# Kernel tuning notes

Measured on AMD Instinct MI355X. Metric: run time of the kernel, lower is better.

## Reference

```python
import jax, jax.numpy as jnp
import numpy as np

EPS = 1e-5
GROUPS = 8


def conv2d(x, w, b, pad):
    y = jax.lax.conv_general_dilated(
        x, w, window_strides=(1, 1), padding=[(pad, pad), (pad, pad)],
        dimension_numbers=('NCHW', 'OIHW', 'NCHW'))
    return y + b[None, :, None, None]


def setup_inputs() -> dict:
    key = jax.random.key(0)
    ks = jax.random.split(key, 8)
    b, c, h, w = 32, 256, 56, 56
    cg = c // GROUPS
    x = jax.random.normal(ks[0], (b, c, h, w), dtype=jnp.float32)
    w1 = jax.random.normal(ks[1], (cg, cg, 1, 1), dtype=jnp.float32) * 0.05
    b1 = jnp.zeros((cg,), dtype=jnp.float32)
    w3a = jax.random.normal(ks[2], (cg, cg, 3, 3), dtype=jnp.float32) * 0.05
    b3a = jnp.zeros((cg,), dtype=jnp.float32)
    w3b = jax.random.normal(ks[3], (c, c, 3, 3), dtype=jnp.float32) * 0.02
    b3b = jnp.zeros((c,), dtype=jnp.float32)
    gn_w = jnp.ones((cg,), dtype=jnp.float32)
    gn_b = jnp.zeros((cg,), dtype=jnp.float32)
    return {"x": x, "w1": w1, "b1": b1, "w3a": w3a, "b3a": b3a,
            "w3b": w3b, "b3b": b3b, "gn_w": gn_w, "gn_b": gn_b}


def reference(x, w1, b1, w3a, b3a, w3b, b3b, gn_w, gn_b):
    b, c, h, w = x.shape
    cg = c // GROUPS
    bg = b * GROUPS
    gx = x.reshape(bg, cg, h, w)

    # spatial attention on grouped channels
    x_h = gx.mean(axis=3, keepdims=True)                       # [bg,cg,h,1]
    x_w = gx.mean(axis=2, keepdims=True).transpose(0, 1, 3, 2)  # [bg,cg,w,1]
    hw = conv2d(jnp.concatenate([x_h, x_w], axis=2), w1, b1, 0)
    xh, xw = hw[:, :, :h], hw[:, :, h:]
    x0 = gx * jax.nn.sigmoid(xh) * jax.nn.sigmoid(xw.transpose(0, 1, 3, 2))

    # GroupNorm with num_groups == num_channels (per-channel over HxW)
    mu = x0.mean(axis=(2, 3), keepdims=True)
    var = x0.var(axis=(2, 3), keepdims=True)
    x1 = (x0 - mu) / jnp.sqrt(var + EPS) * gn_w[None, :, None, None] + gn_b[None, :, None, None]

    x2 = conv2d(gx, w3a, b3a, 1)

    # channel softmax-matmul attention (per group)
    x11 = jax.nn.softmax(x1.mean(axis=(2, 3)), axis=-1)[:, None, :]  # [bg,1,cg]
    x12 = x1.reshape(bg, cg, h * w)
    x21 = jax.nn.softmax(x2.mean(axis=(2, 3)), axis=-1)[:, None, :]
    x22 = x2.reshape(bg, cg, h * w)
    weights1 = (jnp.matmul(x11, x22) + jnp.matmul(x21, x12)).reshape(bg, 1, h, w)

    # BatchNorm2d(affine=False), batch statistics (training mode)
    xr = x0.reshape(b, c, h, w)
    bm = xr.mean(axis=(0, 2, 3), keepdims=True)
    bv = xr.var(axis=(0, 2, 3), keepdims=True)
    x3 = (xr - bm) / jnp.sqrt(bv + EPS)

    x4 = conv2d(x, w3b, b3b, 1)

    # spatial softmax-matmul attention over full channels
    x31 = jax.nn.softmax(x3.mean(axis=1).reshape(b, 1, h * w), axis=-1)  # [b,1,hw]
    x32 = x3.reshape(b, c, h * w).transpose(0, 2, 1)                     # [b,hw,c]
    x41 = jax.nn.softmax(x4.mean(axis=1).reshape(b, 1, h * w), axis=-1)
    x42 = x4.reshape(b, c, h * w).transpose(0, 2, 1)
    weights2 = (jnp.matmul(x31, x42) + jnp.matmul(x41, x32)).reshape(b, c, 1, 1)

    return (gx * jax.nn.sigmoid(weights1)).reshape(b, c, h, w) + x * jax.nn.sigmoid(weights2)
```

## Files before the change

kernel.cpp:

```cpp
#include <hip/hip_runtime.h>
#include <math.h>

#define B  32
#define C  256
#define HH 56
#define WW 56
#define HW 3136
#define G  8
#define CG 32
#define BG 256
#define GC 8192
#define EPSF 1e-5f

typedef __attribute__((ext_vector_type(8))) short short8;
typedef __attribute__((ext_vector_type(4))) float f32x4;

#define GLOAD16(g, l) __builtin_amdgcn_global_load_lds( \
    (const __attribute__((address_space(1))) void*)(g), \
    (__attribute__((address_space(3))) void*)(l), 16, 0, 0)

__device__ __forceinline__ float sigmoidf_(float v){ return 1.0f/(1.0f+__expf(-v)); }
__device__ __forceinline__ unsigned short f2bf(float v){
  unsigned u = __builtin_bit_cast(unsigned, v);
  u = u + 0x7FFFu + ((u>>16)&1u);
  return (unsigned short)(u>>16);
}
__device__ __forceinline__ float bf2f(unsigned short v){
  return __builtin_bit_cast(float, ((unsigned)v)<<16);
}

__global__ __launch_bounds__(256) void k1x(const float* __restrict__ x, unsigned short* __restrict__ xt,
    float* __restrict__ rowm, float* __restrict__ colm){
  int bid = blockIdx.x;
  int b = bid>>4; int icb = (bid>>1)&7; int rh = bid&1;
  __shared__ float tile[32][57];
  __shared__ float colacc[32][56];
  int tid = threadIdx.x;
  for(int e=tid; e<1792; e+=256) colacc[e/56][e%56] = 0.f;
  __syncthreads();
  const float* xb = x + ((size_t)b*256 + icb*32)*HW;
  for(int ii=0; ii<28; ++ii){
    int i = rh*28 + ii;
    for(int e=tid; e<1792; e+=256){
      int ch=e/56, j=e%56;
      tile[ch][j] = xb[(size_t)ch*HW + i*56 + j];
    }
    __syncthreads();
    if(tid<32){
      float s=0.f;
      #pragma unroll 8
      for(int j=0;j<56;j++) s += tile[tid][j];
      rowm[((size_t)b*256 + icb*32 + tid)*56 + i] = s*(1.0f/56.0f);
    }
    for(int e=tid; e<1792; e+=256){
      int ch=e/56, j=e%56;
      colacc[ch][j] += tile[ch][j];
    }
    if(tid<224){
      int j = tid>>2, k = tid&3;
      short8 v;
      #pragma unroll
      for(int m=0;m<8;m++) v[m] = (short)f2bf(tile[k*8+m][j]);
      *(short8*)(xt + (((size_t)b*58 + i+1)*58 + (j+1))*256 + icb*32 + k*8) = v;
    }
    __syncthreads();
  }
  for(int e=tid; e<1792; e+=256){
    int ch=e/56, j=e%56;
    atomicAdd(&colm[((size_t)b*256+icb*32+ch)*56 + j], colacc[ch][j]);
  }
}

__global__ void khalo(unsigned short* __restrict__ xt){
  int bid = blockIdx.x;
  int b = bid/228, hp = bid%228;
  int pi, pj;
  if(hp<58){pi=0;pj=hp;}
  else if(hp<116){pi=57;pj=hp-58;}
  else if(hp<172){pi=hp-116+1;pj=0;}
  else {pi=hp-172+1;pj=57;}
  xt[(((size_t)b*58+pi)*58+pj)*256 + threadIdx.x] = 0;
}

__global__ void k2_hw(const float* __restrict__ rowm, const float* __restrict__ colm,
                      const float* __restrict__ w1, const float* __restrict__ b1,
                      float* __restrict__ sh, float* __restrict__ sw,
                      float* __restrict__ shT, float* __restrict__ swT){
  int bg = blockIdx.x;
  int b = bg>>3, g = bg&7;
  __shared__ float inb[32][112];
  __shared__ float wt[32*32];
  __shared__ float bb[32];
  for(int idx=threadIdx.x; idx<32*56; idx+=blockDim.x){
    int ic=idx/56, p=idx%56;
    inb[ic][p]    = rowm[(bg*32+ic)*56+p];
    inb[ic][56+p] = colm[(bg*32+ic)*56+p]*(1.0f/56.0f);
  }
  for(int idx=threadIdx.x; idx<1024; idx+=blockDim.x) wt[idx]=w1[idx];
  if(threadIdx.x<32) bb[threadIdx.x]=b1[threadIdx.x];
  __syncthreads();
  for(int o=threadIdx.x; o<32*112; o+=blockDim.x){
    int oc=o/112, p=o%112;
    float s=bb[oc];
    #pragma unroll
    for(int ic=0;ic<32;ic++) s += wt[oc*32+ic]*inb[ic][p];
    float sg = sigmoidf_(s);
    int c = g*32+oc;
    if(p<56){
      sh[(bg*32+oc)*56+p]=sg;
      shT[((size_t)b*56+p)*256 + c]=sg;
    } else {
      sw[(bg*32+oc)*56+(p-56)]=sg;
      swT[((size_t)b*56+(p-56))*256 + c]=sg;
    }
  }
}

__global__ void k2b_x11(const float* __restrict__ gnb, const float* __restrict__ b3a, float* __restrict__ x11){
  __shared__ float v[32];
  if(threadIdx.x<32) v[threadIdx.x]=gnb[threadIdx.x];
  __syncthreads();
  if(threadIdx.x==0){
    float m=-1e30f; for(int i=0;i<32;i++) m=fmaxf(m,v[i]);
    float s=0.f; for(int i=0;i<32;i++){ v[i]=__expf(v[i]-m); s+=v[i]; }
    float d=0.f;
    for(int i=0;i<32;i++){ float p=v[i]/s; x11[i]=p; d+=p*b3a[i]; }
    x11[32]=d;
  }
}

__global__ void k3_stats(const float* __restrict__ x, const float* __restrict__ sh, const float* __restrict__ sw,
                         float* __restrict__ gsum, float* __restrict__ gsq){
  int gc=blockIdx.x;
  __shared__ float ssh[56], ssw[56];
  if(threadIdx.x<56) ssh[threadIdx.x]=sh[gc*56+threadIdx.x];
  else if(threadIdx.x>=64&&threadIdx.x<120) ssw[threadIdx.x-64]=sw[gc*56+threadIdx.x-64];
  __syncthreads();
  const float* xp=x+(size_t)gc*HW;
  float s=0.f,s2=0.f;
  for(int p=threadIdx.x;p<HW;p+=blockDim.x){
    float v=xp[p]*ssh[p/56]*ssw[p%56];
    s+=v; s2+=v*v;
  }
  for(int off=32;off>0;off>>=1){ s+=__shfl_down(s,off,64); s2+=__shfl_down(s2,off,64); }
  __shared__ float rs[4], rs2[4];
  int wid=threadIdx.x>>6, lane=threadIdx.x&63;
  if(lane==0){rs[wid]=s; rs2[wid]=s2;}
  __syncthreads();
  if(threadIdx.x==0){
    gsum[gc]=rs[0]+rs[1]+rs[2]+rs[3];
    gsq[gc]=rs2[0]+rs2[1]+rs2[2]+rs2[3];
  }
}

__global__ void k4a(const float* __restrict__ gsum, const float* __restrict__ gsq,
                    float* __restrict__ mu, float* __restrict__ istd){
  int gc=blockIdx.x*256+threadIdx.x;
  float m=gsum[gc]*(1.0f/HW);
  float v=gsq[gc]*(1.0f/HW)-m*m;
  mu[gc]=m; istd[gc]=rsqrtf(v+EPSF);
}

__global__ void k4b(const float* __restrict__ gsum, const float* __restrict__ gsq,
                    float* __restrict__ bm, float* __restrict__ binv){
  int c=threadIdx.x;
  float s=0.f,s2=0.f;
  for(int b=0;b<B;b++){ s+=gsum[b*256+c]; s2+=gsq[b*256+c]; }
  float m=s*(1.0f/(B*HW));
  float v=s2*(1.0f/(B*HW))-m*m;
  bm[c]=m; binv[c]=rsqrtf(v+EPSF);
}

__global__ __launch_bounds__(128) void k5m(const unsigned short* __restrict__ xt,
    const unsigned short* __restrict__ wta, const float* __restrict__ x11,
    float* __restrict__ w1a, float* __restrict__ cs2){
  __shared__ short Bs[6*58*32];
  int bid = blockIdx.x;
  int xcd = bid & 7; int idx = bid >> 3;
  int b = xcd + 8*(idx/112); int idx2 = idx % 112;
  int g = idx2 / 14; int pt = idx2 % 14;
  int bg = b*8 + g;
  int i0 = pt*4;
  int tid = threadIdx.x;
  int lane = tid & 63, wv = tid >> 6;
  int q = lane >> 4, rl = lane & 15;
  const unsigned short* xb = xt + (size_t)b*58*58*256 + g*32;

  #pragma unroll
  for(int issue=0; issue<11; ++issue){
    int idxl = issue*128 + tid;
    if(idxl < 1392){
      int pl = idxl >> 2, ch = idxl & 3;
      int r = pl / 58, jj = pl - r*58;
      const unsigned short* src = xb + ((size_t)(i0 + r)*58 + jj)*256 + ((ch ^ ((pl>>1)&3))<<3);
      GLOAD16(src, &Bs[idxl*8]);
    }
  }
  __syncthreads();

  f32x4 acc[2][7];
  #pragma unroll
  for(int mi=0;mi<2;mi++)
    #pragma unroll
    for(int ni=0;ni<7;ni++) acc[mi][ni]=(f32x4){0.f,0.f,0.f,0.f};

  int pr[7], pj[7];
  #pragma unroll
  for(int ni=0;ni<7;ni++){
    int px = wv*112 + ni*16 + rl;
    pr[ni] = px/56; pj[ni] = px - pr[ni]*56;
  }

  for(int tap=0; tap<9; ++tap){
    int dy = tap/3, dx = tap - dy*3;
    short8 a[2], bfr[7];
    #pragma unroll
    for(int mi=0;mi<2;mi++)
      a[mi] = *(const short8*)(wta + tap*1024 + (mi*16+rl)*32 + q*8);
    #pragma unroll
    for(int ni=0;ni<7;ni++){
      int pix = (pr[ni] + dy)*58 + pj[ni] + dx;
      int cs = q ^ ((pix>>1)&3);
      bfr[ni] = *(const short8*)&Bs[pix*32 + cs*8];
    }
    #pragma unroll
    for(int mi=0;mi<2;mi++)
      #pragma unroll
      for(int ni=0;ni<7;ni++)
        acc[mi][ni] = __builtin_amdgcn_mfma_f32_16x16x32_bf16(a[mi], bfr[ni], acc[mi][ni], 0,0,0);
  }

  float x11v[2][4];
  #pragma unroll
  for(int mi=0;mi<2;mi++)
    #pragma unroll
    for(int r=0;r<4;r++) x11v[mi][r] = x11[mi*16 + q*4 + r];
  float x11b = x11[32];
  size_t pxg0 = (size_t)bg*HW + i0*56 + wv*112;
  #pragma unroll
  for(int ni=0;ni<7;ni++){
    float s=0.f;
    #pragma unroll
    for(int mi=0;mi<2;mi++)
      #pragma unroll
      for(int r=0;r<4;r++) s += x11v[mi][r]*acc[mi][ni][r];
    s += __shfl_xor(s,16,64);
    s += __shfl_xor(s,32,64);
    if(lane<16) w1a[pxg0 + ni*16 + lane] = s + x11b;
  }
  #pragma unroll
  for(int mi=0;mi<2;mi++){
    #pragma unroll
    for(int r=0;r<4;r++){
      float s=0.f;
      #pragma unroll
      for(int ni=0;ni<7;ni++) s += acc[mi][ni][r];
      s += __shfl_xor(s,1,64);
      s += __shfl_xor(s,2,64);
      s += __shfl_xor(s,4,64);
      s += __shfl_xor(s,8,64);
      if(rl==0) atomicAdd(&cs2[bg*32 + mi*16 + q*4 + r], s);
    }
  }
}

__global__ void k6(const float* __restrict__ cs2, const float* __restrict__ b3a,
                   const float* __restrict__ mu, const float* __restrict__ istd,
                   const float* __restrict__ gnw, const float* __restrict__ gnb,
                   float* __restrict__ av, float* __restrict__ cst){
  int bg=blockIdx.x; int t=threadIdx.x;
  float m = cs2[bg*32+t]*(1.0f/HW) + b3a[t];
  float mx=m;
  for(int off=16;off>0;off>>=1) mx=fmaxf(mx,__shfl_xor(mx,off,32));
  float e=__expf(m-mx);
  float s=e;
  for(int off=16;off>0;off>>=1) s+=__shfl_xor(s,off,32);
  float x21=e/s;
  int gc=bg*32+t;
  float is=istd[gc];
  av[gc]=x21*is*gnw[t];
  float cv=x21*(gnb[t]-mu[gc]*is*gnw[t]);
  for(int off=16;off>0;off>>=1) cv+=__shfl_xor(cv,off,32);
  if(t==0) cst[bg]=cv;
}

__global__ __launch_bounds__(256) void k7x(const unsigned short* __restrict__ xt,
    const float* __restrict__ shT, const float* __restrict__ swT,
    const float* __restrict__ av, const float* __restrict__ binv, const float* __restrict__ cst,
    const float* __restrict__ w1a, float* __restrict__ sg1, float* __restrict__ s3pre){
  int bid = blockIdx.x; int b = bid/56, i = bid%56;
  __shared__ float shs[256], avs[256], bins[256], cst8[8];
  int tid = threadIdx.x;
  shs[tid]  = shT[((size_t)b*56+i)*256 + tid];
  avs[tid]  = av[b*256 + tid];
  bins[tid] = binv[tid];
  if(tid<8) cst8[tid] = cst[b*8+tid];
  __syncthreads();
  int h = tid>>5, l = tid&31;
  int bg = l>>2;
  int c0 = l*8;
  float sh8[8], av8[8], bi8[8];
  #pragma unroll
  for(int m=0;m<8;m++){ sh8[m]=shs[c0+m]; av8[m]=avs[c0+m]; bi8[m]=bins[c0+m]; }
  float cstv = cst8[bg];
  for(int pass=0; pass<7; ++pass){
    int j = pass*8 + h;
    short8 xv = *(const short8*)(xt + (((size_t)b*58 + i+1)*58 + j+1)*256 + c0);
    const float* swp = swT + ((size_t)b*56 + j)*256 + c0;
    float ws=0.f, s3=0.f;
    #pragma unroll
    for(int m=0;m<8;m++){
      float x0 = bf2f((unsigned short)xv[m]) * sh8[m] * swp[m];
      ws += av8[m]*x0;
      s3 += bi8[m]*x0;
    }
    ws += __shfl_xor(ws,1,64);
    ws += __shfl_xor(ws,2,64);
    s3 += __shfl_xor(s3,1,64);
    s3 += __shfl_xor(s3,2,64);
    s3 += __shfl_xor(s3,4,64);
    s3 += __shfl_xor(s3,8,64);
    s3 += __shfl_xor(s3,16,64);
    int p = i*56 + j;
    if((l&3)==0){
      size_t o = ((size_t)(b*8+bg))*HW + p;
      sg1[o] = sigmoidf_(w1a[o] + ws + cstv);
    }
    if(l==0) s3pre[(size_t)b*HW + p] = s3*(1.0f/256.0f);
  }
}

__global__ void k_softmax_hw(const float* __restrict__ in, float* __restrict__ out, float scale){
  int b=blockIdx.x;
  const float* ip=in+(size_t)b*HW;
  float mx=-1e30f;
  for(int p=threadIdx.x;p<HW;p+=blockDim.x) mx=fmaxf(mx,ip[p]*scale);
  for(int off=32;off>0;off>>=1) mx=fmaxf(mx,__shfl_xor(mx,off,64));
  __shared__ float red[8];
  int wid=threadIdx.x>>6, lane=threadIdx.x&63;
  if(lane==0) red[wid]=mx;
  __syncthreads();
  mx=red[0];
  #pragma unroll
  for(int w=1;w<8;w++) mx=fmaxf(mx,red[w]);
  float s=0.f;
  for(int p=threadIdx.x;p<HW;p+=blockDim.x) s+=__expf(ip[p]*scale-mx);
  for(int off=32;off>0;off>>=1) s+=__shfl_down(s,off,64);
  __shared__ float red2[8];
  if(lane==0) red2[wid]=s;
  __syncthreads();
  s=red2[0];
  #pragma unroll
  for(int w=1;w<8;w++) s+=red2[w];
  float inv=1.0f/s;
  for(int p=threadIdx.x;p<HW;p+=blockDim.x) out[(size_t)b*HW+p]=__expf(ip[p]*scale-mx)*inv;
}

__global__ void kwt(const float* __restrict__ w3b, unsigned short* __restrict__ wt){
  int idx = blockIdx.x*256 + threadIdx.x;
  int tap = idx >> 16; int r = idx & 65535; int oc = r >> 8; int ic = r & 255;
  wt[idx] = f2bf(w3b[((size_t)oc*256 + ic)*9 + tap]);
}

__global__ void kwta(const float* __restrict__ w3a, unsigned short* __restrict__ wta){
  int idx = blockIdx.x*256 + threadIdx.x;
  if(idx < 9216){
    int tap = idx >> 10; int r = idx & 1023; int oc = r >> 5; int ic = r & 31;
    wta[idx] = f2bf(w3a[((size_t)oc*32 + ic)*9 + tap]);
  }
}

__global__ __launch_bounds__(512) void k9m(const unsigned short* __restrict__ xt,
    const unsigned short* __restrict__ wt, const float* __restrict__ x31,
    float* __restrict__ s4pre, float* __restrict__ w2a){
  __shared__ short Ab[2][128*32];
  __shared__ short Bb[2][224*32];
  int bid = blockIdx.x;
  int xcd = bid & 7; int idx = bid >> 3;
  int b = xcd + 8*(idx/28); int rr = idx % 28;
  int pt = rr >> 1; int oct = rr & 1;
  int i0 = pt*4; int ocb = oct*128;
  int tid = threadIdx.x;
  int lane = tid & 63, wv = tid >> 6;
  int wm = wv & 3, wn = wv >> 2;
  int q = lane >> 4, rl = lane & 15;
  const unsigned short* xb = xt + (size_t)b*58*58*256;

  #define STAGE_A(BUF, TAP, IC0) do{ \
    int idxl = tid; int oc_ = idxl>>2, cs_ = idxl&3; \
    const unsigned short* src = wt + (((size_t)(TAP)*256 + ocb + oc_)*256 + (IC0) + (((cs_ ^ ((oc_>>1)&3)))<<3)); \
    GLOAD16(src, &Ab[BUF][idxl*8]); }while(0)
  #define STAGE_B(BUF, TAP, IC0) do{ \
    int dy_ = (TAP)/3, dx_ = (TAP)%3; \
    { int idxl = tid; int px_ = idxl>>2, cs_ = idxl&3; int r_ = px_/56, j_ = px_ - r_*56; \
      const unsigned short* src = xb + ((size_t)((i0 + r_ + dy_)*58 + (j_ + dx_)))*256 + (IC0) + ((cs_ ^ ((px_>>1)&3))<<3); \
      GLOAD16(src, &Bb[BUF][idxl*8]); } \
    if(tid < 384){ int idxl = tid + 512; int px_ = idxl>>2, cs_ = idxl&3; int r_ = px_/56, j_ = px_ - r_*56; \
      const unsigned short* src = xb + ((size_t)((i0 + r_ + dy_)*58 + (j_ + dx_)))*256 + (IC0) + ((cs_ ^ ((px_>>1)&3))<<3); \
      GLOAD16(src, &Bb[BUF][idxl*8]); } }while(0)

  STAGE_A(0, 0, 0);
  STAGE_B(0, 0, 0);
  __syncthreads();

  f32x4 acc[2][7];
  #pragma unroll
  for(int mi=0;mi<2;mi++)
    #pragma unroll
    for(int ni=0;ni<7;ni++) acc[mi][ni] = (f32x4){0.f,0.f,0.f,0.f};

  for(int t=0; t<72; ++t){
    int cur = t & 1;
    if(t+1 < 72){
      int tn = t+1; int tap = tn >> 3; int ic0 = (tn & 7) << 5;
      STAGE_A(cur^1, tap, ic0);
      STAGE_B(cur^1, tap, ic0);
    }
    short8 a[2], bf[7];
    #pragma unroll
    for(int mi=0;mi<2;mi++){
      int row = wm*32 + mi*16 + rl;
      int cs = q ^ ((row>>1)&3);
      a[mi] = *(const short8*)&Ab[cur][row*32 + cs*8];
    }
    #pragma unroll
    for(int ni=0;ni<7;ni++){
      int px = wn*112 + ni*16 + rl;
      int cs = q ^ ((px>>1)&3);
      bf[ni] = *(const short8*)&Bb[cur][px*32 + cs*8];
    }
    #pragma unroll
    for(int mi=0;mi<2;mi++)
      #pragma unroll
      for(int ni=0;ni<7;ni++)
        acc[mi][ni] = __builtin_amdgcn_mfma_f32_16x16x32_bf16(a[mi], bf[ni], acc[mi][ni], 0,0,0);
    __syncthreads();
  }
  #undef STAGE_A
  #undef STAGE_B

  size_t pxbase = (size_t)b*HW + i0*56 + wn*112;
  #pragma unroll
  for(int ni=0;ni<7;ni++){
    float s = 0.f;
    #pragma unroll
    for(int mi=0;mi<2;mi++){
      s += acc[mi][ni][0]+acc[mi][ni][1]+acc[mi][ni][2]+acc[mi][ni][3];
    }
    s += __shfl_xor(s, 16, 64);
    s += __shfl_xor(s, 32, 64);
    if(lane < 16) atomicAdd(&s4pre[pxbase + ni*16 + lane], s);
  }
  float x31v[7];
  #pragma unroll
  for(int ni=0;ni<7;ni++) x31v[ni] = x31[pxbase + ni*16 + rl];
  #pragma unroll
  for(int mi=0;mi<2;mi++){
    #pragma unroll
    for(int r=0;r<4;r++){
      float s = 0.f;
      #pragma unroll
      for(int ni=0;ni<7;ni++) s += x31v[ni]*acc[mi][ni][r];
      s += __shfl_xor(s, 1, 64);
      s += __shfl_xor(s, 2, 64);
      s += __shfl_xor(s, 4, 64);
      s += __shfl_xor(s, 8, 64);
      if(rl == 0) atomicAdd(&w2a[b*256 + ocb + wm*32 + mi*16 + q*4 + r], s);
    }
  }
}

__global__ __launch_bounds__(256) void k11f(const float* __restrict__ x, const float* __restrict__ sh,
    const float* __restrict__ sw, const float* __restrict__ x41, const float* __restrict__ bm,
    const float* __restrict__ binv, const float* __restrict__ w2a, const float* __restrict__ b3b,
    const float* __restrict__ sg1, float* __restrict__ out){
  int gc=blockIdx.x; int b=gc>>8, c=gc&255, bg=gc>>5;
  __shared__ float xs[HW];
  __shared__ float ssh[56], ssw[56];
  __shared__ float red[4];
  int tid=threadIdx.x;
  if(tid<56) ssh[tid]=sh[gc*56+tid];
  else if(tid>=64&&tid<120) ssw[tid-64]=sw[gc*56+tid-64];
  const float* xp=x+(size_t)gc*HW;
  const float* wp=x41+(size_t)b*HW;
  for(int p=tid;p<HW;p+=256) xs[p]=xp[p];
  __syncthreads();
  float s=0.f;
  for(int p=tid;p<HW;p+=256){
    float x0=xs[p]*ssh[p/56]*ssw[p%56];
    s+=wp[p]*x0;
  }
  for(int off=32;off>0;off>>=1) s+=__shfl_down(s,off,64);
  int wid=tid>>6, lane=tid&63;
  if(lane==0) red[wid]=s;
  __syncthreads();
  float t=red[0]+red[1]+red[2]+red[3];
  float sg2=sigmoidf_(w2a[gc]+b3b[c]+binv[c]*t-bm[c]*binv[c]);
  const float* sp=sg1+(size_t)bg*HW;
  float* op=out+(size_t)gc*HW;
  for(int p=tid;p<HW;p+=256){
    op[p]=xs[p]*(sp[p]+sg2);
  }
}

extern "C" void kernel_launch(void* const* d_in, const int* in_sizes, int n_in,
                              void* d_out, int out_size, void* d_ws, size_t ws_size,
                              hipStream_t stream) {
  const float* x   = (const float*)d_in[0];
  const float* w1  = (const float*)d_in[1];
  const float* b1  = (const float*)d_in[2];
  const float* w3a = (const float*)d_in[3];
  const float* b3a = (const float*)d_in[4];
  const float* w3b = (const float*)d_in[5];
  const float* b3b = (const float*)d_in[6];
  const float* gnw = (const float*)d_in[7];
  const float* gnb = (const float*)d_in[8];
  float* out=(float*)d_out;
  float* ws=(float*)d_ws;

  float* rowm=ws;
  float* colm=rowm+458752;
  float* sh  =colm+458752;
  float* sw  =sh+458752;
  float* x11 =sw+458752;
  float* gsum=x11+64;
  float* gsq =gsum+8192;
  float* mu  =gsq+8192;
  float* istd=mu+8192;
  float* bm  =istd+8192;
  float* binv=bm+256;
  float* cs2 =binv+256;
  float* w1a =cs2+8192;
  float* av  =w1a+802816;
  float* cst =av+8192;
  float* s3  =cst+256;
  float* x31 =s3+100352;
  float* s4  =x31+100352;
  float* x41 =s4+100352;
  float* w2a =x41+100352;
  float* shT =w2a+8192;
  float* swT =shT+458752;
  float* sg1 =swT+458752;
  unsigned short* xt = (unsigned short*)(sg1 + 802816);
  unsigned short* wtb = xt + (size_t)32*58*58*256;
  unsigned short* wta = wtb + 589824;

  hipMemsetAsync(colm, 0, 458752*sizeof(float), stream);
  k1x<<<512,256,0,stream>>>(x, xt, rowm, colm);
  khalo<<<32*228,256,0,stream>>>(xt);
  kwt<<<2304,256,0,stream>>>(w3b, wtb);
  kwta<<<36,256,0,stream>>>(w3a, wta);

  k2_hw<<<BG,128,0,stream>>>(rowm,colm,w1,b1,sh,sw,shT,swT);
  k2b_x11<<<1,32,0,stream>>>(gnb,b3a,x11);
  k3_stats<<<GC,256,0,stream>>>(x,sh,sw,gsum,gsq);
  k4a<<<32,256,0,stream>>>(gsum,gsq,mu,istd);
  k4b<<<1,256,0,stream>>>(gsum,gsq,bm,binv);
  hipMemsetAsync(cs2,0,8192*sizeof(float),stream);
  k5m<<<256*14,128,0,stream>>>(xt,wta,x11,w1a,cs2);
  k6<<<BG,32,0,stream>>>(cs2,b3a,mu,istd,gnw,gnb,av,cst);
  k7x<<<B*56,256,0,stream>>>(xt,shT,swT,av,binv,cst,w1a,sg1,s3);
  k_softmax_hw<<<B,512,0,stream>>>(s3,x31,1.0f);
  hipMemsetAsync(w2a,0,8192*sizeof(float),stream);
  hipMemsetAsync(s4,0,(size_t)HW*B*sizeof(float),stream);
  k9m<<<32*28,512,0,stream>>>(xt,wtb,x31,s4,w2a);
  k_softmax_hw<<<B,512,0,stream>>>(s4,x41,1.0f/256.0f);
  k11f<<<GC,256,0,stream>>>(x,sh,sw,x41,bm,binv,w2a,b3b,sg1,out);
}
```

Baseline: 415.5 us.

## Split fused transpose/row-col-mean kernel into separate highly parallel kernels

Replaces the single 512-block kernel, which looped over rows to build the bf16 NHWC padded copy and row/column means with atomics, with two kernels. A tiled 64x64 transpose kernel launches 6272 blocks to write the bf16 copy, and a per-channel kernel (8192 blocks) computes row and column means directly without atomics or a memset. The aim is more parallelism and no serial loop or atomic traffic, at the cost of reading x twice from memory and scalar 2-byte stores in the transpose.

After: 357.1 us. 1.16x faster.

```diff
diff --git a/kernel.cpp b/kernel.cpp
--- a/kernel.cpp
+++ b/kernel.cpp
@@ -29,45 +29,45 @@
   return __builtin_bit_cast(float, ((unsigned)v)<<16);
 }
 
-__global__ __launch_bounds__(256) void k1x(const float* __restrict__ x, unsigned short* __restrict__ xt,
-    float* __restrict__ rowm, float* __restrict__ colm){
+__global__ void k1_rowcol(const float* __restrict__ x, float* __restrict__ rowm, float* __restrict__ colm){
+  int gc = blockIdx.x;
+  __shared__ float t[56][57];
+  const float* xp = x + (size_t)gc*HW;
+  for(int idx=threadIdx.x; idx<HW; idx+=blockDim.x) t[idx/56][idx%56] = xp[idx];
+  __syncthreads();
+  int tid = threadIdx.x;
+  if(tid < 56){
+    float s=0.f;
+    #pragma unroll 8
+    for(int j=0;j<56;j++) s+=t[tid][j];
+    rowm[gc*56+tid] = s*(1.0f/56.0f);
+  } else if(tid>=64 && tid<120){
+    int j=tid-64; float s=0.f;
+    #pragma unroll 8
+    for(int i=0;i<56;i++) s+=t[i][j];
+    colm[gc*56+j] = s*(1.0f/56.0f);
+  }
+}
+
+__global__ void kxt(const float* __restrict__ x, unsigned short* __restrict__ xt){
   int bid = blockIdx.x;
-  int b = bid>>4; int icb = (bid>>1)&7; int rh = bid&1;
-  __shared__ float tile[32][57];
-  __shared__ float colacc[32][56];
+  int b = bid / 196; int r2 = bid % 196; int icb = r2 / 49; int pxb = r2 % 49;
+  __shared__ float t[64][65];
   int tid = threadIdx.x;
-  for(int e=tid; e<1792; e+=256) colacc[e/56][e%56] = 0.f;
-  __syncthreads();
-  const float* xb = x + ((size_t)b*256 + icb*32)*HW;
-  for(int ii=0; ii<28; ++ii){
-    int i = rh*28 + ii;
-    for(int e=tid; e<1792; e+=256){
-      int ch=e/56, j=e%56;
-      tile[ch][j] = xb[(size_t)ch*HW + i*56 + j];
-    }
-    __syncthreads();
-    if(tid<32){
-      float s=0.f;
-      #pragma unroll 8
-      for(int j=0;j<56;j++) s += tile[tid][j];
-      rowm[((size_t)b*256 + icb*32 + tid)*56 + i] = s*(1.0f/56.0f);
-    }
-    for(int e=tid; e<1792; e+=256){
-      int ch=e/56, j=e%56;
-      colacc[ch][j] += tile[ch][j];
-    }
-    if(tid<224){
-      int j = tid>>2, k = tid&3;
-      short8 v;
-      #pragma unroll
-      for(int m=0;m<8;m++) v[m] = (short)f2bf(tile[k*8+m][j]);
-      *(short8*)(xt + (((size_t)b*58 + i+1)*58 + (j+1))*256 + icb*32 + k*8) = v;
-    }
-    __syncthreads();
-  }
-  for(int e=tid; e<1792; e+=256){
-    int ch=e/56, j=e%56;
-    atomicAdd(&colm[((size_t)b*256+icb*32+ch)*56 + j], colacc[ch][j]);
+  #pragma unroll
+  for(int k=0;k<16;k++){
+    int e = k*256 + tid;
+    int ic = e>>6, px = e&63;
+    t[ic][px] = x[((size_t)(b*256 + icb*64 + ic))*HW + pxb*64 + px];
+  }
+  __syncthreads();
+  #pragma unroll
+  for(int k=0;k<16;k++){
+    int e = k*256 + tid;
+    int px = e>>6, ic = e&63;
+    int pxg = pxb*64 + px;
+    int pi = pxg/56, pj = pxg%56;
+    xt[(((size_t)b*58 + pi + 1)*58 + pj + 1)*256 + icb*64 + ic] = f2bf(t[ic][px]);
   }
 }
 
@@ -94,7 +94,7 @@
   for(int idx=threadIdx.x; idx<32*56; idx+=blockDim.x){
     int ic=idx/56, p=idx%56;
     inb[ic][p]    = rowm[(bg*32+ic)*56+p];
-    inb[ic][56+p] = colm[(bg*32+ic)*56+p]*(1.0f/56.0f);
+    inb[ic][56+p] = colm[(bg*32+ic)*56+p];
   }
   for(int idx=threadIdx.x; idx<1024; idx+=blockDim.x) wt[idx]=w1[idx];
   if(threadIdx.x<32) bb[threadIdx.x]=b1[threadIdx.x];
@@ -545,12 +545,12 @@
   unsigned short* wtb = xt + (size_t)32*58*58*256;
   unsigned short* wta = wtb + 589824;
 
-  hipMemsetAsync(colm, 0, 458752*sizeof(float), stream);
-  k1x<<<512,256,0,stream>>>(x, xt, rowm, colm);
+  kxt<<<32*4*49,256,0,stream>>>(x, xt);
   khalo<<<32*228,256,0,stream>>>(xt);
   kwt<<<2304,256,0,stream>>>(w3b, wtb);
   kwta<<<36,256,0,stream>>>(w3a, wta);
 
+  k1_rowcol<<<GC,256,0,stream>>>(x,rowm,colm);
   k2_hw<<<BG,128,0,stream>>>(rowm,colm,w1,b1,sh,sw,shT,swT);
   k2b_x11<<<1,32,0,stream>>>(gnb,b3a,x11);
   k3_stats<<<GC,256,0,stream>>>(x,sh,sw,gsum,gsq);
```
